# Performance work log

Measured on AMD Instinct MI355X. Metric: run time of the kernel, lower is better.

The kernel has to match this reference:

```python
import jax, jax.numpy as jnp
import numpy as np

N = 30000        # nodes
E = 480000       # edges
IN_DIM = 128
HID = 64
OUT = 64
POS_DIM = 32
H = 4            # heads (same for all layers)
PVOCAB = 3
NEG_SLOPE = 0.2


def _xavier(key, shape):
    fan_in, fan_out = shape[0], shape[-1] if len(shape) > 1 else shape[0]
    scale = 1.414 * np.sqrt(2.0 / (fan_in + fan_out))
    return jax.random.normal(key, shape, dtype=jnp.float32) * scale


def setup_inputs() -> dict:
    key = jax.random.key(0)
    ks = jax.random.split(key, 20)
    d0_in = IN_DIM + POS_DIM            # 160
    d_mid = HID * H + POS_DIM           # 288
    inp = {
        "features": jax.random.normal(ks[0], (N, IN_DIM), dtype=jnp.float32),
        # layer 0
        "W0": _xavier(ks[1], (d0_in, H * HID)),
        "al0": _xavier(ks[2], (H, HID)),
        "ar0": _xavier(ks[3], (H, HID)),
        "pe0": _xavier(ks[4], (PVOCAB, POS_DIM)),
        # layer 1
        "W1": _xavier(ks[5], (d_mid, H * HID)),
        "al1": _xavier(ks[6], (H, HID)),
        "ar1": _xavier(ks[7], (H, HID)),
        "pe1": _xavier(ks[8], (PVOCAB, POS_DIM)),
        # output layer
        "W2": _xavier(ks[9], (d_mid, H * OUT)),
        "al2": _xavier(ks[10], (H, OUT)),
        "ar2": _xavier(ks[11], (H, OUT)),
        "pe2": _xavier(ks[12], (PVOCAB, POS_DIM)),
        # graph
        "src": jax.random.randint(ks[13], (E,), 0, N, dtype=jnp.int32),
        "dst": jax.random.randint(ks[14], (E,), 0, N, dtype=jnp.int32),
        "pos": jax.random.randint(ks[15], (N,), 0, PVOCAB, dtype=jnp.int32),
    }
    return inp


def gat_layer(h, W, a_l, a_r, src, dst):
    # h: [N, in_d]; W: [in_d, H*d]; a_l,a_r: [H, d]
    n = h.shape[0]
    nh, d = a_l.shape
    ft = (h @ W).reshape(n, nh, d)                       # [N,H,d]
    a1 = jnp.einsum("nhd,hd->nh", ft, a_l)               # [N,H]
    a2 = jnp.einsum("nhd,hd->nh", ft, a_r)               # [N,H]
    e = jax.nn.leaky_relu(a1[src] + a2[dst], NEG_SLOPE)  # [E,H]
    # per-destination segment softmax (numerically stable)
    m = jax.ops.segment_max(e, dst, num_segments=n)      # [N,H]
    ex = jnp.exp(e - m[dst])                             # [E,H]
    s = jax.ops.segment_sum(ex, dst, num_segments=n)     # [N,H]
    alpha = ex / s[dst]                                  # [E,H]
    msg = ft[src] * alpha[:, :, None]                    # [E,H,d]
    return jax.ops.segment_sum(msg, dst, num_segments=n) # [N,H,d]


def reference(features, W0, al0, ar0, pe0, W1, al1, ar1, pe1,
              W2, al2, ar2, pe2, src, dst, pos):
    h = features
    # hidden GAT layers with ELU activation and head-flattening
    for W, al, ar, pe in ((W0, al0, ar0, pe0), (W1, al1, ar1, pe1)):
        p = pe[pos]                                      # [N, pos_dim]
        hcat = jnp.concatenate((h, p), axis=1)
        out = gat_layer(hcat, W, al, ar, src, dst)       # [N,H,d]
        h = jax.nn.elu(out.reshape(out.shape[0], -1))    # [N,H*d]
    # output layer: mean over heads
    p = pe2[pos]
    hcat = jnp.concatenate((h, p), axis=1)
    out = gat_layer(hcat, W2, al2, ar2, src, dst)        # [N,H,out]
    return out.mean(axis=1)                              # [N,out]
```

## Files before the change

kernel.cpp:

```cpp
#include <hip/hip_runtime.h>
#include <hip/hip_fp16.h>
#include <math.h>

#define N_NODES 30000
#define N_EDGES 480000
#define HEADS 4
#define DHEAD 64
#define FDIM 256
#define POSD 32
#define SCAN_B 1024
#define SCAN_NB ((N_NODES + SCAN_B - 1) / SCAN_B)

typedef _Float16 half8 __attribute__((ext_vector_type(8)));
typedef float floatx4 __attribute__((ext_vector_type(4)));

__device__ __forceinline__ float lrelu(float x){ return x > 0.f ? x : 0.2f * x; }

__global__ void hist_k(const int* __restrict__ dst, int* __restrict__ deg){
  int e = blockIdx.x * blockDim.x + threadIdx.x;
  if (e < N_EDGES) atomicAdd(&deg[dst[e]], 1);
}

__global__ void scanA_k(const int* __restrict__ deg, int* __restrict__ off,
                        int* __restrict__ bsum){
  __shared__ int sm[SCAN_B];
  int t = threadIdx.x;
  int i = blockIdx.x * SCAN_B + t;
  int x = (i < N_NODES) ? deg[i] : 0;
  sm[t] = x;
  __syncthreads();
#pragma unroll
  for (int o = 1; o < SCAN_B; o <<= 1){
    int v = (t >= o) ? sm[t - o] : 0;
    __syncthreads();
    sm[t] += v;
    __syncthreads();
  }
  if (i < N_NODES) off[i] = sm[t] - x;
  if (t == SCAN_B - 1) bsum[blockIdx.x] = sm[t];
}

__global__ void scanB_k(int* __restrict__ bsum, int* __restrict__ boff){
  __shared__ int sm[64];
  int t = threadIdx.x;
  int x = (t < SCAN_NB) ? bsum[t] : 0;
  sm[t] = x;
  __syncthreads();
#pragma unroll
  for (int o = 1; o < 64; o <<= 1){
    int v = (t >= o) ? sm[t - o] : 0;
    __syncthreads();
    sm[t] += v;
    __syncthreads();
  }
  if (t < SCAN_NB) boff[t] = sm[t] - x;
}

__global__ void scanC_k(int* __restrict__ off, const int* __restrict__ boff,
                        int* __restrict__ cursor){
  int i = blockIdx.x * SCAN_B + threadIdx.x;
  if (i < N_NODES){
    int v = off[i] + boff[blockIdx.x];
    off[i] = v;
    cursor[i] = v;
  }
  if (i == 0) off[N_NODES] = N_EDGES;
}

__global__ void scatter_k(const int* __restrict__ src, const int* __restrict__ dst,
                          int* __restrict__ cursor, int* __restrict__ esrc){
  int e = blockIdx.x * blockDim.x + threadIdx.x;
  if (e < N_EDGES){
    int d = dst[e];
    int p = atomicAdd(&cursor[d], 1);
    esrc[p] = src[e];
  }
}

__global__ void pw_k(const float* __restrict__ W0, const float* __restrict__ W1,
                     const float* __restrict__ W2, const float* __restrict__ pe0,
                     const float* __restrict__ pe1, const float* __restrict__ pe2,
                     float* __restrict__ PW){
  int layer = blockIdx.x / 3, v = blockIdx.x % 3;
  const float* W  = layer == 0 ? W0 : (layer == 1 ? W1 : W2);
  const float* pe = layer == 0 ? pe0 : (layer == 1 ? pe1 : pe2);
  int K = layer == 0 ? 128 : 256;
  int j = threadIdx.x;
  float s = 0.f;
#pragma unroll
  for (int k = 0; k < POSD; k++)
    s = fmaf(pe[v * POSD + k], W[(size_t)(K + k) * FDIM + j], s);
  PW[(layer * 3 + v) * FDIM + j] = s;
}

__global__ void f2h_k(const float* __restrict__ in, _Float16* __restrict__ out,
                      int n){
  int i = (blockIdx.x * blockDim.x + threadIdx.x) * 4;
  if (i < n){
    float4 v = *(const float4*)&in[i];
    struct h4s { _Float16 h[4]; } u;
    u.h[0] = (_Float16)v.x; u.h[1] = (_Float16)v.y;
    u.h[2] = (_Float16)v.z; u.h[3] = (_Float16)v.w;
    *(h4s*)&out[i] = u;
  }
}

__global__ void wcvt_k(const float* __restrict__ W0, const float* __restrict__ W1,
                       const float* __restrict__ W2, _Float16* __restrict__ T0,
                       _Float16* __restrict__ T1, _Float16* __restrict__ T2){
  int l = blockIdx.y;
  const float* W = l == 0 ? W0 : (l == 1 ? W1 : W2);
  _Float16* T    = l == 0 ? T0 : (l == 1 ? T1 : T2);
  int K = l == 0 ? 128 : 256;
  int n = threadIdx.x;
  for (int k = blockIdx.x; k < K; k += gridDim.x)
    T[(size_t)n * K + k] = (_Float16)W[(size_t)k * FDIM + n];
}

__global__ __launch_bounds__(256) void gemm_mfma_k(
    const _Float16* __restrict__ A, const _Float16* __restrict__ Wt,
    const float* __restrict__ PW, const int* __restrict__ pos,
    const float* __restrict__ al, const float* __restrict__ arw,
    _Float16* __restrict__ Ch, float* __restrict__ a1, float* __restrict__ a2,
    int K){
  int t = threadIdx.x;
  int w = t >> 6;
  int lane = t & 63;
  int lm = lane & 15;
  int kq = lane >> 4;
  int h = blockIdx.x;
  int rowBase = blockIdx.y * 128 + w * 32;
  int colBase = h * 64;

  floatx4 acc[2][4] = {};

  int r0 = min(rowBase + lm, N_NODES - 1);
  int r1 = min(rowBase + 16 + lm, N_NODES - 1);
  const _Float16* Ar0 = A + (size_t)r0 * K;
  const _Float16* Ar1 = A + (size_t)r1 * K;
  const _Float16* B0 = Wt + (size_t)(colBase + 0 * 16 + lm) * K;
  const _Float16* B1 = Wt + (size_t)(colBase + 1 * 16 + lm) * K;
  const _Float16* B2 = Wt + (size_t)(colBase + 2 * 16 + lm) * K;
  const _Float16* B3 = Wt + (size_t)(colBase + 3 * 16 + lm) * K;

  for (int kb = 0; kb < K; kb += 32){
    int ko = kb + kq * 8;
    half8 a0 = *(const half8*)(Ar0 + ko);
    half8 a1f = *(const half8*)(Ar1 + ko);
    half8 b0 = *(const half8*)(B0 + ko);
    half8 b1 = *(const half8*)(B1 + ko);
    half8 b2 = *(const half8*)(B2 + ko);
    half8 b3 = *(const half8*)(B3 + ko);
    acc[0][0] = __builtin_amdgcn_mfma_f32_16x16x32_f16(a0, b0, acc[0][0], 0, 0, 0);
    acc[0][1] = __builtin_amdgcn_mfma_f32_16x16x32_f16(a0, b1, acc[0][1], 0, 0, 0);
    acc[0][2] = __builtin_amdgcn_mfma_f32_16x16x32_f16(a0, b2, acc[0][2], 0, 0, 0);
    acc[0][3] = __builtin_amdgcn_mfma_f32_16x16x32_f16(a0, b3, acc[0][3], 0, 0, 0);
    acc[1][0] = __builtin_amdgcn_mfma_f32_16x16x32_f16(a1f, b0, acc[1][0], 0, 0, 0);
    acc[1][1] = __builtin_amdgcn_mfma_f32_16x16x32_f16(a1f, b1, acc[1][1], 0, 0, 0);
    acc[1][2] = __builtin_amdgcn_mfma_f32_16x16x32_f16(a1f, b2, acc[1][2], 0, 0, 0);
    acc[1][3] = __builtin_amdgcn_mfma_f32_16x16x32_f16(a1f, b3, acc[1][3], 0, 0, 0);
  }

  float alw[4], arr[4];
#pragma unroll
  for (int j = 0; j < 4; j++){
    alw[j] = al [h * DHEAD + j * 16 + lm];
    arr[j] = arw[h * DHEAD + j * 16 + lm];
  }

#pragma unroll
  for (int i = 0; i < 2; i++){
#pragma unroll
    for (int p = 0; p < 4; p++){
      int row = rowBase + i * 16 + kq * 4 + p;
      if (row >= N_NODES) continue;
      int pz = pos[row];
      const float* pwb = PW + pz * FDIM + colBase;
      float s1 = 0.f, s2 = 0.f;
#pragma unroll
      for (int j = 0; j < 4; j++){
        float v = acc[i][j][p] + pwb[j * 16 + lm];
        Ch[(size_t)row * FDIM + colBase + j * 16 + lm] = (_Float16)v;
        s1 = fmaf(v, alw[j], s1);
        s2 = fmaf(v, arr[j], s2);
      }
      s1 += __shfl_xor(s1, 1, 64); s2 += __shfl_xor(s2, 1, 64);
      s1 += __shfl_xor(s1, 2, 64); s2 += __shfl_xor(s2, 2, 64);
      s1 += __shfl_xor(s1, 4, 64); s2 += __shfl_xor(s2, 4, 64);
      s1 += __shfl_xor(s1, 8, 64); s2 += __shfl_xor(s2, 8, 64);
      if (lm == 0){
        a1[row * HEADS + h] = s1;
        a2[row * HEADS + h] = s2;
      }
    }
  }
}

__global__ __launch_bounds__(256) void agg4_k(
    const _Float16* __restrict__ ft, const float* __restrict__ a1,
    const float* __restrict__ a2, const int* __restrict__ off,
    const int* __restrict__ esrc, _Float16* __restrict__ outh,
    float* __restrict__ outf, int mode){
  int wv = threadIdx.x >> 6;
  int lane = threadIdx.x & 63;
  int n = blockIdx.x * 4 + wv;
  if (n >= N_NODES) return;
  int jb = off[n];
  int deg = off[n + 1] - jb;
  int eidx = lane & 15, h = lane >> 4;
  int hsel = h << 4;
  float a2n = a2[n * HEADS + h];
  float4 acc = make_float4(0.f, 0.f, 0.f, 0.f);
  const _Float16* ftl = ft + lane * 4;

  if (deg <= 64){
    int sreg[4]; float wreg[4];
    float m = -INFINITY;
#pragma unroll
    for (int r = 0; r < 4; r++){
      int idx = eidx + r * 16;
      int s = (idx < deg) ? esrc[jb + idx] : 0;
      sreg[r] = s;
      float e = (idx < deg) ? lrelu(a1[s * HEADS + h] + a2n) : -INFINITY;
      wreg[r] = e;
      m = fmaxf(m, e);
    }
    m = fmaxf(m, __shfl_xor(m, 1, 64));
    m = fmaxf(m, __shfl_xor(m, 2, 64));
    m = fmaxf(m, __shfl_xor(m, 4, 64));
    m = fmaxf(m, __shfl_xor(m, 8, 64));
    float ss = 0.f;
#pragma unroll
    for (int r = 0; r < 4; r++){
      int idx = eidx + r * 16;
      float t = (idx < deg) ? __expf(wreg[r] - m) : 0.f;
      wreg[r] = t;
      ss += t;
    }
    ss += __shfl_xor(ss, 1, 64);
    ss += __shfl_xor(ss, 2, 64);
    ss += __shfl_xor(ss, 4, 64);
    ss += __shfl_xor(ss, 8, 64);
    float inv = (ss > 0.f) ? 1.f / ss : 0.f;
#pragma unroll
    for (int r = 0; r < 4; r++) wreg[r] *= inv;

#pragma unroll
    for (int r = 0; r < 4; r++){
      if (r * 16 >= deg) break;
      int lim = deg - r * 16; if (lim > 16) lim = 16;
      float wr = wreg[r]; int sr = sreg[r];
      for (int jj = 0; jj < lim; jj += 4){
#pragma unroll
        for (int u = 0; u < 4; u++){
          float wj = __shfl(wr, (jj + u) | hsel, 64);
          int sj = __shfl(sr, jj + u, 64);
          struct h4 { __half2 a, b; };
          h4 f = *(const h4*)(ftl + (size_t)sj * FDIM);
          float2 fa = __half22float2(f.a), fb = __half22float2(f.b);
          acc.x = fmaf(wj, fa.x, acc.x);
          acc.y = fmaf(wj, fa.y, acc.y);
          acc.z = fmaf(wj, fb.x, acc.z);
          acc.w = fmaf(wj, fb.y, acc.w);
        }
      }
    }
  } else {
    float m = -INFINITY;
    for (int idx = eidx; idx < deg; idx += 16){
      int s = esrc[jb + idx];
      m = fmaxf(m, lrelu(a1[s * HEADS + h] + a2n));
    }
    m = fmaxf(m, __shfl_xor(m, 1, 64));
    m = fmaxf(m, __shfl_xor(m, 2, 64));
    m = fmaxf(m, __shfl_xor(m, 4, 64));
    m = fmaxf(m, __shfl_xor(m, 8, 64));
    float ss = 0.f;
    for (int idx = eidx; idx < deg; idx += 16){
      int s = esrc[jb + idx];
      ss += __expf(lrelu(a1[s * HEADS + h] + a2n) - m);
    }
    ss += __shfl_xor(ss, 1, 64);
    ss += __shfl_xor(ss, 2, 64);
    ss += __shfl_xor(ss, 4, 64);
    ss += __shfl_xor(ss, 8, 64);
    float inv = (ss > 0.f) ? 1.f / ss : 0.f;
    for (int j = 0; j < deg; j++){
      int sj = esrc[jb + j];
      float e = lrelu(a1[sj * HEADS + h] + a2n);
      float wj = __expf(e - m) * inv;
      struct h4 { __half2 a, b; };
      h4 f = *(const h4*)(ftl + (size_t)sj * FDIM);
      float2 fa = __half22float2(f.a), fb = __half22float2(f.b);
      acc.x = fmaf(wj, fa.x, acc.x);
      acc.y = fmaf(wj, fa.y, acc.y);
      acc.z = fmaf(wj, fb.x, acc.z);
      acc.w = fmaf(wj, fb.y, acc.w);
    }
  }

  if (mode == 0){
    acc.x = acc.x > 0.f ? acc.x : (__expf(acc.x) - 1.f);
    acc.y = acc.y > 0.f ? acc.y : (__expf(acc.y) - 1.f);
    acc.z = acc.z > 0.f ? acc.z : (__expf(acc.z) - 1.f);
    acc.w = acc.w > 0.f ? acc.w : (__expf(acc.w) - 1.f);
    struct h4s { _Float16 h[4]; } u;
    u.h[0] = (_Float16)acc.x; u.h[1] = (_Float16)acc.y;
    u.h[2] = (_Float16)acc.z; u.h[3] = (_Float16)acc.w;
    *(h4s*)&outh[(size_t)n * FDIM + lane * 4] = u;
  } else {
#pragma unroll
    for (int o2 = 16; o2 <= 32; o2 <<= 1){
      acc.x += __shfl_xor(acc.x, o2, 64);
      acc.y += __shfl_xor(acc.y, o2, 64);
      acc.z += __shfl_xor(acc.z, o2, 64);
      acc.w += __shfl_xor(acc.w, o2, 64);
    }
    if (lane < 16){
      float4 o;
      o.x = acc.x * 0.25f; o.y = acc.y * 0.25f;
      o.z = acc.z * 0.25f; o.w = acc.w * 0.25f;
      *(float4*)&outf[(size_t)n * DHEAD + lane * 4] = o;
    }
  }
}

extern "C" void kernel_launch(void* const* d_in, const int* in_sizes, int n_in,
                              void* d_out, int out_size, void* d_ws, size_t ws_size,
                              hipStream_t stream){
  const float* features = (const float*)d_in[0];
  const float* W0  = (const float*)d_in[1];
  const float* al0 = (const float*)d_in[2];
  const float* ar0 = (const float*)d_in[3];
  const float* pe0 = (const float*)d_in[4];
  const float* W1  = (const float*)d_in[5];
  const float* al1 = (const float*)d_in[6];
  const float* ar1 = (const float*)d_in[7];
  const float* pe1 = (const float*)d_in[8];
  const float* W2  = (const float*)d_in[9];
  const float* al2 = (const float*)d_in[10];
  const float* ar2 = (const float*)d_in[11];
  const float* pe2 = (const float*)d_in[12];
  const int* srcv  = (const int*)d_in[13];
  const int* dstv  = (const int*)d_in[14];
  const int* posv  = (const int*)d_in[15];
  float* out = (float*)d_out;

  char* wp = (char*)d_ws;
  auto alloc = [&](size_t bytes){
    void* p = (void*)wp;
    wp += (bytes + 255) & ~(size_t)255;
    return p;
  };
  _Float16* fth   = (_Float16*)alloc(sizeof(_Float16) * (size_t)N_NODES * FDIM);
  _Float16* hbuf  = (_Float16*)alloc(sizeof(_Float16) * (size_t)N_NODES * FDIM);
  _Float16* feat16= (_Float16*)alloc(sizeof(_Float16) * (size_t)N_NODES * 128);
  _Float16* Wt0   = (_Float16*)alloc(sizeof(_Float16) * 256 * 128);
  _Float16* Wt1   = (_Float16*)alloc(sizeof(_Float16) * 256 * 256);
  _Float16* Wt2   = (_Float16*)alloc(sizeof(_Float16) * 256 * 256);
  float* a1     = (float*)alloc(sizeof(float) * N_NODES * HEADS);
  float* a2     = (float*)alloc(sizeof(float) * N_NODES * HEADS);
  float* PW     = (float*)alloc(sizeof(float) * 9 * FDIM);
  int*   deg    = (int*)alloc(sizeof(int) * N_NODES);
  int*   off    = (int*)alloc(sizeof(int) * (N_NODES + 1));
  int*   cursor = (int*)alloc(sizeof(int) * N_NODES);
  int*   bsum   = (int*)alloc(sizeof(int) * 64);
  int*   boff   = (int*)alloc(sizeof(int) * 64);
  int*   esrc   = (int*)alloc(sizeof(int) * N_EDGES);

  hipMemsetAsync(deg, 0, sizeof(int) * N_NODES, stream);
  hist_k<<<(N_EDGES + 255) / 256, 256, 0, stream>>>(dstv, deg);
  scanA_k<<<SCAN_NB, SCAN_B, 0, stream>>>(deg, off, bsum);
  scanB_k<<<1, 64, 0, stream>>>(bsum, boff);
  scanC_k<<<SCAN_NB, SCAN_B, 0, stream>>>(off, boff, cursor);
  scatter_k<<<(N_EDGES + 255) / 256, 256, 0, stream>>>(srcv, dstv, cursor, esrc);

  pw_k<<<9, 256, 0, stream>>>(W0, W1, W2, pe0, pe1, pe2, PW);
  f2h_k<<<(N_NODES * 128 / 4 + 255) / 256, 256, 0, stream>>>(
      features, feat16, N_NODES * 128);
  wcvt_k<<<dim3(64, 3), 256, 0, stream>>>(W0, W1, W2, Wt0, Wt1, Wt2);

  dim3 ggrid(HEADS, (N_NODES + 127) / 128);
  int agrid = (N_NODES + 3) / 4;

  gemm_mfma_k<<<ggrid, 256, 0, stream>>>(feat16, Wt0, PW + 0 * 3 * FDIM, posv,
                                         al0, ar0, fth, a1, a2, 128);
  agg4_k<<<agrid, 256, 0, stream>>>(fth, a1, a2, off, esrc, hbuf, nullptr, 0);

  gemm_mfma_k<<<ggrid, 256, 0, stream>>>(hbuf, Wt1, PW + 1 * 3 * FDIM, posv,
                                         al1, ar1, fth, a1, a2, 256);
  agg4_k<<<agrid, 256, 0, stream>>>(fth, a1, a2, off, esrc, hbuf, nullptr, 0);

  gemm_mfma_k<<<ggrid, 256, 0, stream>>>(hbuf, Wt2, PW + 2 * 3 * FDIM, posv,
                                         al2, ar2, fth, a1, a2, 256);
  agg4_k<<<agrid, 256, 0, stream>>>(fth, a1, a2, off, esrc, nullptr, out, 1);
}
```

Measured before the change: 334.0 us.

## Fuse CSR build into one persistent kernel, merge prep kernels, enlarge GEMM tile

Replaces the memset, histogram, three scan kernels and scatter with a single persistent kernel of 60 blocks that separates its phases with an atomic-counter grid barrier. The feature conversion, weight transpose and positional-projection kernels are merged into one launch that branches on block index. The GEMM now gives each wave 64 rows instead of 32, reusing each loaded B fragment across four A fragments. The aim is fewer launches and fewer redundant B loads. The risks are that the spin barrier relies on all 60 blocks being resident at once, the CSR phases get less parallelism, and the larger accumulator raises register pressure.

```diff
diff --git a/kernel.cpp b/kernel.cpp
--- a/kernel.cpp
+++ b/kernel.cpp
@@ -8,113 +8,127 @@
 #define DHEAD 64
 #define FDIM 256
 #define POSD 32
-#define SCAN_B 1024
-#define SCAN_NB ((N_NODES + SCAN_B - 1) / SCAN_B)
+#define CSR_NB 60
+#define SCAN_NB 30
 
 typedef _Float16 half8 __attribute__((ext_vector_type(8)));
 typedef float floatx4 __attribute__((ext_vector_type(4)));
 
 __device__ __forceinline__ float lrelu(float x){ return x > 0.f ? x : 0.2f * x; }
 
-__global__ void hist_k(const int* __restrict__ dst, int* __restrict__ deg){
-  int e = blockIdx.x * blockDim.x + threadIdx.x;
-  if (e < N_EDGES) atomicAdd(&deg[dst[e]], 1);
-}
-
-__global__ void scanA_k(const int* __restrict__ deg, int* __restrict__ off,
-                        int* __restrict__ bsum){
-  __shared__ int sm[SCAN_B];
-  int t = threadIdx.x;
-  int i = blockIdx.x * SCAN_B + t;
-  int x = (i < N_NODES) ? deg[i] : 0;
-  sm[t] = x;
+__device__ __forceinline__ void gridbar(int* bar, int target){
   __syncthreads();
-#pragma unroll
-  for (int o = 1; o < SCAN_B; o <<= 1){
-    int v = (t >= o) ? sm[t - o] : 0;
+  __threadfence();
+  if (threadIdx.x == 0){
+    atomicAdd(bar, 1);
+    while (atomicAdd(bar, 0) < target) { }
+    __threadfence();
+  }
+  __syncthreads();
+}
+
+__global__ __launch_bounds__(1024) void csr_k(
+    const int* __restrict__ src, const int* __restrict__ dst,
+    int* __restrict__ deg, int* __restrict__ off, int* __restrict__ cursor,
+    int* __restrict__ esrc, int* __restrict__ bar, int* __restrict__ bsum,
+    int* __restrict__ boff){
+  __shared__ int sm[1024];
+  int b = blockIdx.x, t = threadIdx.x;
+  int gid = b * 1024 + t, gsz = CSR_NB * 1024;
+
+  for (int i = gid; i < N_NODES; i += gsz) deg[i] = 0;
+  gridbar(bar, 1 * CSR_NB);
+
+  for (int e = gid; e < N_EDGES; e += gsz) atomicAdd(&deg[dst[e]], 1);
+  gridbar(bar, 2 * CSR_NB);
+
+  if (b < SCAN_NB){
+    int i = b * 1024 + t;
+    int x = (i < N_NODES) ? deg[i] : 0;
+    sm[t] = x;
     __syncthreads();
-    sm[t] += v;
+#pragma unroll
+    for (int o = 1; o < 1024; o <<= 1){
+      int v = (t >= o) ? sm[t - o] : 0;
+      __syncthreads();
+      sm[t] += v;
+      __syncthreads();
+    }
+    if (i < N_NODES) off[i] = sm[t] - x;
+    if (t == 1023) bsum[b] = sm[t];
+  }
+  gridbar(bar, 3 * CSR_NB);
+
+  if (b == 0){
+    int x = (t < SCAN_NB) ? bsum[t] : 0;
+    sm[t] = x;
     __syncthreads();
-  }
-  if (i < N_NODES) off[i] = sm[t] - x;
-  if (t == SCAN_B - 1) bsum[blockIdx.x] = sm[t];
-}
-
-__global__ void scanB_k(int* __restrict__ bsum, int* __restrict__ boff){
-  __shared__ int sm[64];
-  int t = threadIdx.x;
-  int x = (t < SCAN_NB) ? bsum[t] : 0;
-  sm[t] = x;
-  __syncthreads();
-#pragma unroll
-  for (int o = 1; o < 64; o <<= 1){
-    int v = (t >= o) ? sm[t - o] : 0;
-    __syncthreads();
-    sm[t] += v;
-    __syncthreads();
-  }
-  if (t < SCAN_NB) boff[t] = sm[t] - x;
-}
-
-__global__ void scanC_k(int* __restrict__ off, const int* __restrict__ boff,
-                        int* __restrict__ cursor){
-  int i = blockIdx.x * SCAN_B + threadIdx.x;
-  if (i < N_NODES){
-    int v = off[i] + boff[blockIdx.x];
-    off[i] = v;
-    cursor[i] = v;
-  }
-  if (i == 0) off[N_NODES] = N_EDGES;
-}
-
-__global__ void scatter_k(const int* __restrict__ src, const int* __restrict__ dst,
-                          int* __restrict__ cursor, int* __restrict__ esrc){
-  int e = blockIdx.x * blockDim.x + threadIdx.x;
-  if (e < N_EDGES){
+#pragma unroll
+    for (int o = 1; o < 64; o <<= 1){
+      int v = (t >= o && t < 64) ? sm[t - o] : 0;
+      __syncthreads();
+      if (t < 64) sm[t] += v;
+      __syncthreads();
+    }
+    if (t < SCAN_NB) boff[t] = sm[t] - x;
+  }
+  gridbar(bar, 4 * CSR_NB);
+
+  if (b < SCAN_NB){
+    int i = b * 1024 + t;
+    if (i < N_NODES){
+      int v = off[i] + boff[b];
+      off[i] = v;
+      cursor[i] = v;
+    }
+  }
+  if (gid == 0) off[N_NODES] = N_EDGES;
+  gridbar(bar, 5 * CSR_NB);
+
+  for (int e = gid; e < N_EDGES; e += gsz){
     int d = dst[e];
     int p = atomicAdd(&cursor[d], 1);
     esrc[p] = src[e];
   }
 }
 
-__global__ void pw_k(const float* __restrict__ W0, const float* __restrict__ W1,
-                     const float* __restrict__ W2, const float* __restrict__ pe0,
-                     const float* __restrict__ pe1, const float* __restrict__ pe2,
-                     float* __restrict__ PW){
-  int layer = blockIdx.x / 3, v = blockIdx.x % 3;
-  const float* W  = layer == 0 ? W0 : (layer == 1 ? W1 : W2);
-  const float* pe = layer == 0 ? pe0 : (layer == 1 ? pe1 : pe2);
-  int K = layer == 0 ? 128 : 256;
-  int j = threadIdx.x;
-  float s = 0.f;
-#pragma unroll
-  for (int k = 0; k < POSD; k++)
-    s = fmaf(pe[v * POSD + k], W[(size_t)(K + k) * FDIM + j], s);
-  PW[(layer * 3 + v) * FDIM + j] = s;
-}
-
-__global__ void f2h_k(const float* __restrict__ in, _Float16* __restrict__ out,
-                      int n){
-  int i = (blockIdx.x * blockDim.x + threadIdx.x) * 4;
-  if (i < n){
-    float4 v = *(const float4*)&in[i];
+__global__ __launch_bounds__(256) void prep_k(
+    const float* __restrict__ features, _Float16* __restrict__ feat16,
+    const float* __restrict__ W0, const float* __restrict__ W1,
+    const float* __restrict__ W2, _Float16* __restrict__ T0,
+    _Float16* __restrict__ T1, _Float16* __restrict__ T2,
+    const float* __restrict__ pe0, const float* __restrict__ pe1,
+    const float* __restrict__ pe2, float* __restrict__ PW){
+  int blk = blockIdx.x;
+  if (blk < 3750){
+    int i = (blk * 256 + threadIdx.x) * 4;
+    float4 v = *(const float4*)&features[i];
     struct h4s { _Float16 h[4]; } u;
     u.h[0] = (_Float16)v.x; u.h[1] = (_Float16)v.y;
     u.h[2] = (_Float16)v.z; u.h[3] = (_Float16)v.w;
-    *(h4s*)&out[i] = u;
-  }
-}
-
-__global__ void wcvt_k(const float* __restrict__ W0, const float* __restrict__ W1,
-                       const float* __restrict__ W2, _Float16* __restrict__ T0,
-                       _Float16* __restrict__ T1, _Float16* __restrict__ T2){
-  int l = blockIdx.y;
-  const float* W = l == 0 ? W0 : (l == 1 ? W1 : W2);
-  _Float16* T    = l == 0 ? T0 : (l == 1 ? T1 : T2);
-  int K = l == 0 ? 128 : 256;
-  int n = threadIdx.x;
-  for (int k = blockIdx.x; k < K; k += gridDim.x)
-    T[(size_t)n * K + k] = (_Float16)W[(size_t)k * FDIM + n];
+    *(h4s*)&feat16[i] = u;
+  } else if (blk < 3942){
+    int q = blk - 3750;
+    int l = q >> 6, kk0 = q & 63;
+    const float* W = l == 0 ? W0 : (l == 1 ? W1 : W2);
+    _Float16* T    = l == 0 ? T0 : (l == 1 ? T1 : T2);
+    int K = l == 0 ? 128 : 256;
+    int n = threadIdx.x;
+    for (int k = kk0; k < K; k += 64)
+      T[(size_t)n * K + k] = (_Float16)W[(size_t)k * FDIM + n];
+  } else {
+    int q = blk - 3942;
+    int layer = q / 3, v = q % 3;
+    const float* W  = layer == 0 ? W0 : (layer == 1 ? W1 : W2);
+    const float* pe = layer == 0 ? pe0 : (layer == 1 ? pe1 : pe2);
+    int K = layer == 0 ? 128 : 256;
+    int j = threadIdx.x;
+    float s = 0.f;
+#pragma unroll
+    for (int k = 0; k < POSD; k++)
+      s = fmaf(pe[v * POSD + k], W[(size_t)(K + k) * FDIM + j], s);
+    PW[(layer * 3 + v) * FDIM + j] = s;
+  }
 }
 
 __global__ __launch_bounds__(256) void gemm_mfma_k(
@@ -129,15 +143,15 @@
   int lm = lane & 15;
   int kq = lane >> 4;
   int h = blockIdx.x;
-  int rowBase = blockIdx.y * 128 + w * 32;
+  int rowBase = blockIdx.y * 256 + w * 64;
   int colBase = h * 64;
 
-  floatx4 acc[2][4] = {};
-
-  int r0 = min(rowBase + lm, N_NODES - 1);
-  int r1 = min(rowBase + 16 + lm, N_NODES - 1);
-  const _Float16* Ar0 = A + (size_t)r0 * K;
-  const _Float16* Ar1 = A + (size_t)r1 * K;
+  floatx4 acc[4][4] = {};
+
+  const _Float16* Ar[4];
+#pragma unroll
+  for (int r = 0; r < 4; r++)
+    Ar[r] = A + (size_t)min(rowBase + r * 16 + lm, N_NODES - 1) * K;
   const _Float16* B0 = Wt + (size_t)(colBase + 0 * 16 + lm) * K;
   const _Float16* B1 = Wt + (size_t)(colBase + 1 * 16 + lm) * K;
   const _Float16* B2 = Wt + (size_t)(colBase + 2 * 16 + lm) * K;
@@ -145,20 +159,18 @@
 
   for (int kb = 0; kb < K; kb += 32){
     int ko = kb + kq * 8;
-    half8 a0 = *(const half8*)(Ar0 + ko);
-    half8 a1f = *(const half8*)(Ar1 + ko);
     half8 b0 = *(const half8*)(B0 + ko);
     half8 b1 = *(const half8*)(B1 + ko);
     half8 b2 = *(const half8*)(B2 + ko);
     half8 b3 = *(const half8*)(B3 + ko);
-    acc[0][0] = __builtin_amdgcn_mfma_f32_16x16x32_f16(a0, b0, acc[0][0], 0, 0, 0);
-    acc[0][1] = __builtin_amdgcn_mfma_f32_16x16x32_f16(a0, b1, acc[0][1], 0, 0, 0);
-    acc[0][2] = __builtin_amdgcn_mfma_f32_16x16x32_f16(a0, b2, acc[0][2], 0, 0, 0);
-    acc[0][3] = __builtin_amdgcn_mfma_f32_16x16x32_f16(a0, b3, acc[0][3], 0, 0, 0);
-    acc[1][0] = __builtin_amdgcn_mfma_f32_16x16x32_f16(a1f, b0, acc[1][0], 0, 0, 0);
-    acc[1][1] = __builtin_amdgcn_mfma_f32_16x16x32_f16(a1f, b1, acc[1][1], 0, 0, 0);
-    acc[1][2] = __builtin_amdgcn_mfma_f32_16x16x32_f16(a1f, b2, acc[1][2], 0, 0, 0);
-    acc[1][3] = __builtin_amdgcn_mfma_f32_16x16x32_f16(a1f, b3, acc[1][3], 0, 0, 0);
+#pragma unroll
+    for (int r = 0; r < 4; r++){
+      half8 af = *(const half8*)(Ar[r] + ko);
+      acc[r][0] = __builtin_amdgcn_mfma_f32_16x16x32_f16(af, b0, acc[r][0], 0, 0, 0);
+      acc[r][1] = __builtin_amdgcn_mfma_f32_16x16x32_f16(af, b1, acc[r][1], 0, 0, 0);
+      acc[r][2] = __builtin_amdgcn_mfma_f32_16x16x32_f16(af, b2, acc[r][2], 0, 0, 0);
+      acc[r][3] = __builtin_amdgcn_mfma_f32_16x16x32_f16(af, b3, acc[r][3], 0, 0, 0);
+    }
   }
 
   float alw[4], arr[4];
@@ -169,17 +181,17 @@
   }
 
 #pragma unroll
-  for (int i = 0; i < 2; i++){
+  for (int r = 0; r < 4; r++){
 #pragma unroll
     for (int p = 0; p < 4; p++){
-      int row = rowBase + i * 16 + kq * 4 + p;
+      int row = rowBase + r * 16 + kq * 4 + p;
       if (row >= N_NODES) continue;
       int pz = pos[row];
       const float* pwb = PW + pz * FDIM + colBase;
       float s1 = 0.f, s2 = 0.f;
 #pragma unroll
       for (int j = 0; j < 4; j++){
-        float v = acc[i][j][p] + pwb[j * 16 + lm];
+        float v = acc[r][j][p] + pwb[j * 16 + lm];
         Ch[(size_t)row * FDIM + colBase + j * 16 + lm] = (_Float16)v;
         s1 = fmaf(v, alw[j], s1);
         s2 = fmaf(v, arr[j], s2);
@@ -233,9 +245,9 @@
 #pragma unroll
     for (int r = 0; r < 4; r++){
       int idx = eidx + r * 16;
-      float t = (idx < deg) ? __expf(wreg[r] - m) : 0.f;
-      wreg[r] = t;
-      ss += t;
+      float tv = (idx < deg) ? __expf(wreg[r] - m) : 0.f;
+      wreg[r] = tv;
+      ss += tv;
     }
     ss += __shfl_xor(ss, 1, 64);
     ss += __shfl_xor(ss, 2, 64);
@@ -366,21 +378,18 @@
   int*   cursor = (int*)alloc(sizeof(int) * N_NODES);
   int*   bsum   = (int*)alloc(sizeof(int) * 64);
   int*   boff   = (int*)alloc(sizeof(int) * 64);
+  int*   bar    = (int*)alloc(sizeof(int) * 64);
   int*   esrc   = (int*)alloc(sizeof(int) * N_EDGES);
 
-  hipMemsetAsync(deg, 0, sizeof(int) * N_NODES, stream);
-  hist_k<<<(N_EDGES + 255) / 256, 256, 0, stream>>>(dstv, deg);
-  scanA_k<<<SCAN_NB, SCAN_B, 0, stream>>>(deg, off, bsum);
-  scanB_k<<<1, 64, 0, stream>>>(bsum, boff);
-  scanC_k<<<SCAN_NB, SCAN_B, 0, stream>>>(off, boff, cursor);
-  scatter_k<<<(N_EDGES + 255) / 256, 256, 0, stream>>>(srcv, dstv, cursor, esrc);
-
-  pw_k<<<9, 256, 0, stream>>>(W0, W1, W2, pe0, pe1, pe2, PW);
-  f2h_k<<<(N_NODES * 128 / 4 + 255) / 256, 256, 0, stream>>>(
-      features, feat16, N_NODES * 128);
-  wcvt_k<<<dim3(64, 3), 256, 0, stream>>>(W0, W1, W2, Wt0, Wt1, Wt2);
-
-  dim3 ggrid(HEADS, (N_NODES + 127) / 128);
+  hipMemsetAsync(bar, 0, sizeof(int), stream);
+
+  csr_k<<<CSR_NB, 1024, 0, stream>>>(srcv, dstv, deg, off, cursor, esrc,
+                                     bar, bsum, boff);
+
+  prep_k<<<3951, 256, 0, stream>>>(features, feat16, W0, W1, W2,
+                                   Wt0, Wt1, Wt2, pe0, pe1, pe2, PW);
+
+  dim3 ggrid(HEADS, (N_NODES + 255) / 256);
   int agrid = (N_NODES + 3) / 4;
 
   gemm_mfma_k<<<ggrid, 256, 0, stream>>>(feat16, Wt0, PW + 0 * 3 * FDIM, posv,
```

Result: slower. 399.7 us (+19.7%).
